# Optimization experiments

Hardware: AMD Instinct MI355X
Metric: run time of the kernel (lower is better)

## Reference

```python
import jax, jax.numpy as jnp
import numpy as np

B, L = 2, 2048
IN_DIM, HD_DIM, STATE_DIM = 512, 4096, 16
NUM_PATHS, ENT_DEPTH = 2, 2
ENT_STRENGTH, WALK_TIME = 0.3, 1.0


def _glorot(key, shape):
    lim = np.sqrt(6.0 / (shape[0] + shape[1]))
    return jax.random.uniform(key, shape, jnp.float32, -lim, lim)


def setup_inputs() -> dict:
    key = jax.random.key(0)
    ks = jax.random.split(key, 10)
    x = jax.random.normal(ks[0], (B, L, IN_DIM), jnp.float32)
    input_proj = _glorot(ks[1], (IN_DIM, HD_DIM))
    output_proj = _glorot(ks[2], (HD_DIM, IN_DIM))
    a_log = jax.random.uniform(ks[3], (STATE_DIM,), jnp.float32, -4.0, -1.0)
    b_proj = _glorot(ks[4], (HD_DIM, STATE_DIM))
    c_proj = _glorot(ks[5], (HD_DIM, STATE_DIM))
    dt_proj = jnp.full((HD_DIM,), 0.01, jnp.float32)
    skip_proj = jnp.ones((HD_DIM,), jnp.float32)  # diagonal skip, init 1.0
    amplitudes_real = jnp.full((NUM_PATHS,), 1.0 / np.sqrt(NUM_PATHS), jnp.float32)
    amplitudes_imag = 0.01 * jax.random.normal(ks[6], (NUM_PATHS,), jnp.float32)
    rotation_angles = jax.random.uniform(ks[7], (ENT_DEPTH, NUM_PATHS), jnp.float32, 0.0, 2.0 * np.pi)
    wh, _ = jnp.linalg.qr(jax.random.normal(ks[8], (NUM_PATHS, NUM_PATHS), jnp.float32))  # orthogonal init
    return dict(x=x, input_proj=input_proj, output_proj=output_proj, a_log=a_log,
                b_proj=b_proj, c_proj=c_proj, dt_proj=dt_proj, skip_proj=skip_proj,
                amplitudes_real=amplitudes_real, amplitudes_imag=amplitudes_imag,
                rotation_angles=rotation_angles, walk_hamiltonian=wh)


def _qhd_forward(x, input_proj, output_proj, a_log, b_proj, c_proj, dt_proj,
                 skip_proj, amp_r, amp_i, rot, walk_h):
    Bb, Ll, _ = x.shape
    K = amp_r.shape[0]
    dt = jax.nn.softplus(dt_proj)                                   # (D,)
    hd = jnp.einsum('bld,dh->blh', x, input_proj)                   # (B,L,D)
    # --- frequency-stratified superposition paths (K bands) ---
    Xf = jnp.fft.rfft(hd, axis=1)                                   # (B,F,D) complex
    F = Xf.shape[1]
    band = jnp.clip(jnp.arange(F) * K // F, 0, K - 1)
    masks = (band[None, :] == jnp.arange(K)[:, None]).astype(hd.dtype)  # (K,F)
    x_paths = jnp.fft.irfft(Xf[None] * masks[:, None, :, None], n=Ll, axis=2)  # (K,B,L,D)
    # --- FFT-domain diagonal selective SSM (causal conv with exp decay) ---
    a = -jnp.exp(a_log)                                             # (N,)
    dt_bar = jnp.mean(dt)
    t_idx = jnp.arange(Ll, dtype=hd.dtype)
    decay = jnp.exp(a[None, :] * dt_bar * t_idx[:, None])           # (L,N)
    Bt = jnp.einsum('kbld,dn->kbln', x_paths * dt, b_proj)          # (K,B,L,N)
    n2 = 2 * Ll
    h = jnp.fft.irfft(jnp.fft.rfft(Bt, n=n2, axis=2) * jnp.fft.rfft(decay, n=n2, axis=0),
                      n=n2, axis=2)[:, :, :Ll, :]                   # (K,B,L,N)
    y_paths = jnp.einsum('kbln,dn->kbld', h, c_proj)                # (K,B,L,D)
    # --- VQC entanglement (RY-style phase + quantum-walk mixing) ---
    alpha = amp_r.astype(jnp.complex64) + 1j * amp_i.astype(jnp.complex64)
    A = 1j * (ENT_STRENGTH * WALK_TIME) * walk_h.astype(jnp.complex64)
    U = jnp.eye(K, dtype=jnp.complex64) + A + (A @ A) / 2.0 + (A @ A @ A) / 6.0
    for d in range(rot.shape[0]):
        alpha = jnp.exp(1j * rot[d].astype(jnp.complex64)) * alpha
        alpha = U @ alpha
    # --- Born rule collapse ---
    w = jnp.abs(alpha) ** 2
    w = (w / jnp.sum(w)).astype(hd.dtype)                           # (K,)
    y = jnp.einsum('k,kbld->bld', w, y_paths) + hd * skip_proj      # diagonal skip
    return jnp.einsum('blh,hd->bld', y, output_proj)                # (B,L,in_dim)


def reference(x, input_proj, output_proj, a_log, b_proj, c_proj, dt_proj,
              skip_proj, amplitudes_real, amplitudes_imag, rotation_angles,
              walk_hamiltonian):
    return _qhd_forward(x, input_proj, output_proj, a_log, b_proj, c_proj,
                        dt_proj, skip_proj, amplitudes_real, amplitudes_imag,
                        rotation_angles, walk_hamiltonian)
```

## Files before the change

### kernel.cpp

```cpp
#include <hip/hip_runtime.h>
#include <cstdint>

typedef unsigned short ushort_t;
typedef __bf16 bf16x8 __attribute__((ext_vector_type(8)));
typedef float f32x4 __attribute__((ext_vector_type(4)));

#define PI_F 3.14159265358979323846f

__device__ __forceinline__ ushort_t f2bf(float f) {
  uint32_t x = __float_as_uint(f);
  x += 0x7fffu + ((x >> 16) & 1u);
  return (ushort_t)(x >> 16);
}
__device__ __forceinline__ float bf2f(ushort_t u) {
  return __uint_as_float(((uint32_t)u) << 16);
}
__device__ __forceinline__ float softplusf(float x) {
  return (x > 20.f) ? x : log1pf(expf(x));
}
__device__ __forceinline__ void async_ld16(ushort_t* lds, const ushort_t* g) {
  __builtin_amdgcn_global_load_lds(
      (const __attribute__((address_space(1))) uint32_t*)g,
      (__attribute__((address_space(3))) uint32_t*)lds, 16, 0, 0);
}
__device__ __forceinline__ void load16f(const float* p, float* v) {
  const float4* q = reinterpret_cast<const float4*>(p);
  float4 t0 = q[0], t1 = q[1], t2 = q[2], t3 = q[3];
  v[0]=t0.x; v[1]=t0.y; v[2]=t0.z; v[3]=t0.w;
  v[4]=t1.x; v[5]=t1.y; v[6]=t1.z; v[7]=t1.w;
  v[8]=t2.x; v[9]=t2.y; v[10]=t2.z; v[11]=t2.w;
  v[12]=t3.x; v[13]=t3.y; v[14]=t3.z; v[15]=t3.w;
}


__global__ __launch_bounds__(256) void cast_bf16(const float* __restrict__ in,
                                                 ushort_t* __restrict__ out, int n) {
  int i = blockIdx.x * 256 + threadIdx.x;
  if (i < n) out[i] = f2bf(in[i]);
}

__global__ __launch_bounds__(256) void zero_f4(float4* __restrict__ p) {
  int i = blockIdx.x * 256 + threadIdx.x;
  p[i] = (float4){0.f, 0.f, 0.f, 0.f};
}

__global__ __launch_bounds__(256) void transpose_cast(const float* __restrict__ in,
                                                      ushort_t* __restrict__ out,
                                                      int R, int C,
                                                      const float* __restrict__ scale) {
  __shared__ float t[32][33];
  int bc = blockIdx.x * 32;
  int br = blockIdx.y * 32;
  int tx = threadIdx.x, ty = threadIdx.y;
#pragma unroll
  for (int i = ty; i < 32; i += 8)
    t[i][tx] = in[(size_t)(br + i) * C + bc + tx];
  __syncthreads();
#pragma unroll
  for (int i = ty; i < 32; i += 8) {
    float sv = scale ? scale[bc + i] : 1.f;
    out[(size_t)(bc + i) * R + br + tx] = f2bf(t[tx][i] * sv);
  }
}

__global__ __launch_bounds__(256) void bdt_kernel(const float* __restrict__ bp,
                                                  const float* __restrict__ dtp,
                                                  float* __restrict__ bdt) {
  int i = blockIdx.x * 256 + threadIdx.x;
  bdt[i] = bp[i] * softplusf(dtp[i >> 4]);
}

__global__ __launch_bounds__(256) void small_setup(const float* __restrict__ dtp,
                                                   const float* __restrict__ a_log,
                                                   const float* __restrict__ ar,
                                                   const float* __restrict__ ai,
                                                   const float* __restrict__ rot,
                                                   const float* __restrict__ wh,
                                                   float* __restrict__ sc) {
  __shared__ float red[256];
  float s = 0.f;
  for (int i = threadIdx.x; i < 4096; i += 256) s += softplusf(dtp[i]);
  red[threadIdx.x] = s;
  __syncthreads();
  for (int st = 128; st > 0; st >>= 1) {
    if (threadIdx.x < st) red[threadIdx.x] += red[threadIdx.x + st];
    __syncthreads();
  }
  if (threadIdx.x == 0) {
    float dtbar = red[0] / 4096.f;
    float B00 = 0.3f * wh[0], B01 = 0.3f * wh[1], B10 = 0.3f * wh[2], B11 = 0.3f * wh[3];
    float C00 = B00*B00 + B01*B10, C01 = B00*B01 + B01*B11;
    float C10 = B10*B00 + B11*B10, C11 = B10*B01 + B11*B11;
    float D00 = C00*B00 + C01*B10, D01 = C00*B01 + C01*B11;
    float D10 = C10*B00 + C11*B10, D11 = C10*B01 + C11*B11;
    float Ur00 = 1.f - 0.5f*C00, Ur01 = -0.5f*C01, Ur10 = -0.5f*C10, Ur11 = 1.f - 0.5f*C11;
    float Ui00 = B00 - D00/6.f, Ui01 = B01 - D01/6.f, Ui10 = B10 - D10/6.f, Ui11 = B11 - D11/6.f;
    float a0r = ar[0], a0i = ai[0], a1r = ar[1], a1i = ai[1];
#pragma unroll
    for (int d = 0; d < 2; ++d) {
      float c0 = cosf(rot[d*2+0]), s0 = sinf(rot[d*2+0]);
      float c1 = cosf(rot[d*2+1]), s1 = sinf(rot[d*2+1]);
      float t0r = a0r*c0 - a0i*s0, t0i = a0r*s0 + a0i*c0;
      float t1r = a1r*c1 - a1i*s1, t1i = a1r*s1 + a1i*c1;
      a0r = Ur00*t0r - Ui00*t0i + Ur01*t1r - Ui01*t1i;
      a0i = Ur00*t0i + Ui00*t0r + Ur01*t1i + Ui01*t1r;
      a1r = Ur10*t0r - Ui10*t0i + Ur11*t1r - Ui11*t1i;
      a1i = Ur10*t0i + Ui10*t0r + Ur11*t1i + Ui11*t1r;
    }
    float p0 = a0r*a0r + a0i*a0i, p1 = a1r*a1r + a1i*a1i;
    float inv = 1.f / (p0 + p1);
    sc[0] = p0 * inv; sc[1] = p1 * inv; sc[2] = dtbar;
#pragma unroll
    for (int n = 0; n < 16; ++n) {
      float a = -expf(a_log[n]);
      sc[8 + n]  = expf(a * dtbar);
      sc[24 + n] = expf(a * dtbar * 32.f);
    }
  }
}


__global__ __launch_bounds__(256)
void skinny16(const float* __restrict__ A, const float* __restrict__ Bm,
              float* __restrict__ C, int K, int lda) {
  const int m0 = blockIdx.x << 2;
  const int tid = threadIdx.x;
  float acc[4][16];
#pragma unroll
  for (int a = 0; a < 4; ++a)
#pragma unroll
    for (int n = 0; n < 16; ++n) acc[a][n] = 0.f;

  for (int d = tid; d < K; d += 256) {
    float bv[16];
    load16f(Bm + (size_t)d * 16, bv);
    float av[4];
#pragma unroll
    for (int a = 0; a < 4; ++a) av[a] = A[(size_t)(m0 + a) * lda + d];
#pragma unroll
    for (int a = 0; a < 4; ++a)
#pragma unroll
      for (int n = 0; n < 16; ++n) acc[a][n] += av[a] * bv[n];
  }
  __shared__ float sred[4][4][16];
  const int w = tid >> 6, lane = tid & 63;
#pragma unroll
  for (int a = 0; a < 4; ++a)
#pragma unroll
    for (int n = 0; n < 16; ++n) {
      float v = acc[a][n];
#pragma unroll
      for (int off2 = 32; off2 > 0; off2 >>= 1) v += __shfl_down(v, off2);
      if (lane == 0) sred[w][a][n] = v;
    }
  __syncthreads();
  if (tid < 64) {
    int a = tid >> 4, n = tid & 15;
    C[(size_t)(m0 + a) * 16 + n] =
        sred[0][a][n] + sred[1][a][n] + sred[2][a][n] + sred[3][a][n];
  }
}


template<int BM, int BN, int WR, int WC, bool OBF, bool FUSE>
__global__ __launch_bounds__(256)
void gemm_bf16(const ushort_t* __restrict__ A, const ushort_t* __restrict__ Bt,
               void* __restrict__ Cv, int M, int N, int Kc, int lda, int ldb, int swz,
               const ushort_t* __restrict__ hb, const ushort_t* __restrict__ cp) {
  constexpr int BK = 64;
  constexpr int WMR = BM / WR;
  constexpr int WNC = BN / WC;
  constexpr int MI = WMR / 16;
  constexpr int NI = WNC / 16;
  constexpr int NCA = BM * BK * 2 / 1024;
  constexpr int NCB = BN * BK * 2 / 1024;

  __shared__ ushort_t lA[BM * BK];
  __shared__ ushort_t lB[BN * BK];

  const int tid = threadIdx.x;
  const int w = tid >> 6, lane = tid & 63;
  const int wr = w / WC, wc = w % WC;
  const int r = lane & 15, g = lane >> 4;

  const int nbx = gridDim.x;
  int bid = blockIdx.y * nbx + blockIdx.x;
  if (swz) {
    const int nwg = nbx * gridDim.y;
    bid = (bid & 7) * (nwg >> 3) + (bid >> 3);
  }
  const int m0 = (bid / nbx) * BM, n0 = (bid % nbx) * BN;
  const int kz = blockIdx.z * Kc;

  f32x4 acc[MI][NI];
#pragma unroll
  for (int mi = 0; mi < MI; ++mi)
#pragma unroll
    for (int ni = 0; ni < NI; ++ni)
      acc[mi][ni] = (f32x4){0.f, 0.f, 0.f, 0.f};

  const int ktiles = Kc >> 6;
  for (int kt = 0; kt < ktiles; ++kt) {
    const int k0 = kz + (kt << 6);
    for (int c = w; c < NCA; c += 4) {
      int byteoff = (c << 10) + (lane << 4);
      int row = byteoff >> 7;
      int scol = (byteoff & 127) ^ ((row & 7) << 4);
      async_ld16(&lA[c << 9], &A[(size_t)(m0 + row) * lda + k0 + (scol >> 1)]);
    }
    for (int c = w; c < NCB; c += 4) {
      int byteoff = (c << 10) + (lane << 4);
      int row = byteoff >> 7;
      int scol = (byteoff & 127) ^ ((row & 7) << 4);
      async_ld16(&lB[c << 9], &Bt[(size_t)(n0 + row) * ldb + k0 + (scol >> 1)]);
    }
    __syncthreads();
#pragma unroll
    for (int kk = 0; kk < 2; ++kk) {
      bf16x8 av[MI], bv[NI];
#pragma unroll
      for (int mi = 0; mi < MI; ++mi) {
        int row = wr * WMR + mi * 16 + r;
        int off = (((kk << 2) + g) ^ (row & 7)) << 3;
        av[mi] = *reinterpret_cast<const bf16x8*>(&lA[row * 64 + off]);
      }
#pragma unroll
      for (int ni = 0; ni < NI; ++ni) {
        int row = wc * WNC + ni * 16 + r;
        int off = (((kk << 2) + g) ^ (row & 7)) << 3;
        bv[ni] = *reinterpret_cast<const bf16x8*>(&lB[row * 64 + off]);
      }
#pragma unroll
      for (int mi = 0; mi < MI; ++mi)
#pragma unroll
        for (int ni = 0; ni < NI; ++ni)
          acc[mi][ni] = __builtin_amdgcn_mfma_f32_16x16x32_bf16(av[mi], bv[ni], acc[mi][ni], 0, 0, 0);
    }
    __syncthreads();
  }

  if constexpr (FUSE) {
    bf16x8 zv;
#pragma unroll
    for (int t2 = 0; t2 < 8; ++t2) zv[t2] = (__bf16)0.0f;
    bf16x8 ah[MI], bh[NI];
#pragma unroll
    for (int mi = 0; mi < MI; ++mi) {
      ah[mi] = zv;
      if (g < 2) {
        int row = m0 + wr * WMR + mi * 16 + r;
        ah[mi] = *reinterpret_cast<const bf16x8*>(&hb[(size_t)row * 16 + g * 8]);
      }
    }
#pragma unroll
    for (int ni = 0; ni < NI; ++ni) {
      bh[ni] = zv;
      if (g < 2) {
        int col = n0 + wc * WNC + ni * 16 + r;
        bh[ni] = *reinterpret_cast<const bf16x8*>(&cp[(size_t)col * 16 + g * 8]);
      }
    }
#pragma unroll
    for (int mi = 0; mi < MI; ++mi)
#pragma unroll
      for (int ni = 0; ni < NI; ++ni)
        acc[mi][ni] = __builtin_amdgcn_mfma_f32_16x16x32_bf16(ah[mi], bh[ni], acc[mi][ni], 0, 0, 0);
  }

#pragma unroll
  for (int mi = 0; mi < MI; ++mi)
#pragma unroll
    for (int ni = 0; ni < NI; ++ni) {
      int row = m0 + wr * WMR + mi * 16 + g * 4;
      int col = n0 + wc * WNC + ni * 16 + r;
#pragma unroll
      for (int j = 0; j < 4; ++j) {
        size_t idx = (size_t)(row + j) * N + col;
        if (OBF) ((ushort_t*)Cv)[idx] = f2bf(acc[mi][ni][j]);
        else     unsafeAtomicAdd(&((float*)Cv)[idx], acc[mi][ni][j]);
      }
    }
}


__global__ __launch_bounds__(256)
void freq_ssm(const float* __restrict__ Bhd, const float* __restrict__ sc,
              ushort_t* __restrict__ h) {
  const int blk = blockIdx.x;
  const int b = blk >> 4, n = blk & 15;
  const int tid = threadIdx.x;
  __shared__ float2 X[2048];
  __shared__ float carr[64], pre[64];
  const float w0 = sc[0], w1 = sc[1];
  const float r = sc[8 + n], r32 = sc[24 + n];

  for (int l = tid; l < 2048; l += 256) {
    X[l].x = Bhd[(size_t)(b * 2048 + l) * 16 + n];
    X[l].y = 0.f;
  }
  for (int ls = 10; ls >= 0; --ls) {
    int s = 1 << ls;
    __syncthreads();
    for (int q = tid; q < 1024; q += 256) {
      int j = q & (s - 1);
      int base = (q >> ls) << (ls + 1);
      int i0 = base + j, i1 = i0 + s;
      float2 a = X[i0], bb = X[i1];
      X[i0].x = a.x + bb.x; X[i0].y = a.y + bb.y;
      float tx = a.x - bb.x, ty = a.y - bb.y;
      float ang = -PI_F * (float)j / (float)s;
      float sn, cs; sincosf(ang, &sn, &cs);
      X[i1].x = tx * cs - ty * sn;
      X[i1].y = tx * sn + ty * cs;
    }
  }
  __syncthreads();
  for (int i = tid; i < 2048; i += 256) {
    unsigned f = __brev((unsigned)i) >> 21;
    float wv = (f <= 512u || f >= 1536u) ? w0 : w1;
    X[i].x *= wv; X[i].y *= wv;
  }
  for (int ls = 0; ls <= 10; ++ls) {
    int s = 1 << ls;
    __syncthreads();
    for (int q = tid; q < 1024; q += 256) {
      int j = q & (s - 1);
      int base = (q >> ls) << (ls + 1);
      int i0 = base + j, i1 = i0 + s;
      float ang = PI_F * (float)j / (float)s;
      float sn, cs; sincosf(ang, &sn, &cs);
      float2 bb = X[i1];
      float bx = bb.x * cs - bb.y * sn;
      float by = bb.x * sn + bb.y * cs;
      float2 a = X[i0];
      X[i0].x = a.x + bx; X[i0].y = a.y + by;
      X[i1].x = a.x - bx; X[i1].y = a.y - by;
    }
  }
  __syncthreads();
  const float inv = 1.0f / 2048.0f;
  if (tid < 64) {
    float c = 0.f;
    int base = tid * 32;
#pragma unroll
    for (int i = 0; i < 32; ++i) c = r * c + X[base + i].x * inv;
    carr[tid] = c;
  }
  __syncthreads();
  if (tid == 0) {
    float s = 0.f;
    for (int j2 = 0; j2 < 64; ++j2) { pre[j2] = s; s = s * r32 + carr[j2]; }
  }
  __syncthreads();
  if (tid < 64) {
    float s = pre[tid];
    int base = tid * 32;
#pragma unroll
    for (int i = 0; i < 32; ++i) {
      s = r * s + X[base + i].x * inv;
      h[(size_t)(b * 2048 + base + i) * 16 + n] = f2bf(s);
    }
  }
}


extern "C" void kernel_launch(void* const* d_in, const int* in_sizes, int n_in,
                              void* d_out, int out_size, void* d_ws, size_t ws_size,
                              hipStream_t stream) {
  (void)in_sizes; (void)n_in; (void)out_size; (void)ws_size;
  const float* x      = (const float*)d_in[0];
  const float* Win    = (const float*)d_in[1];
  const float* Wout   = (const float*)d_in[2];
  const float* a_log  = (const float*)d_in[3];
  const float* b_proj = (const float*)d_in[4];
  const float* c_proj = (const float*)d_in[5];
  const float* dt_proj= (const float*)d_in[6];
  const float* skip   = (const float*)d_in[7];
  const float* ampr   = (const float*)d_in[8];
  const float* ampi   = (const float*)d_in[9];
  const float* rot    = (const float*)d_in[10];
  const float* wh     = (const float*)d_in[11];
  float* out = (float*)d_out;

  char* ws = (char*)d_ws;
  ushort_t* A1  = (ushort_t*)(ws + 0);
  ushort_t* Wt1 = (ushort_t*)(ws + 4194304);
  ushort_t* Wt2 = (ushort_t*)(ws + 8388608);
  float*    bdt = (float*)(ws + 12582912);
  float*    Wb  = (float*)(ws + 12845056);
  float*    Bhd = (float*)(ws + 12910592);
  ushort_t* hb  = (ushort_t*)(ws + 13172736);
  ushort_t* cp16= (ushort_t*)(ws + 13303808);
  float*    sc  = (float*)(ws + 13434880);
  ushort_t* y   = (ushort_t*)(ws + 13435136);

  zero_f4<<<2048, 256, 0, stream>>>((float4*)out);
  cast_bf16<<<8192, 256, 0, stream>>>(x, A1, 4096 * 512);
  cast_bf16<<<256, 256, 0, stream>>>(c_proj, cp16, 65536);
  transpose_cast<<<dim3(128, 16), dim3(32, 8), 0, stream>>>(Win, Wt1, 512, 4096, skip);
  transpose_cast<<<dim3(16, 128), dim3(32, 8), 0, stream>>>(Wout, Wt2, 4096, 512, nullptr);
  bdt_kernel<<<256, 256, 0, stream>>>(b_proj, dt_proj, bdt);
  small_setup<<<1, 256, 0, stream>>>(dt_proj, a_log, ampr, ampi, rot, wh, sc);

  skinny16<<<128, 256, 0, stream>>>(Win, bdt, Wb, 4096, 4096);
  skinny16<<<1024, 256, 0, stream>>>(x, Wb, Bhd, 512, 512);
  freq_ssm<<<32, 256, 0, stream>>>(Bhd, sc, hb);

  gemm_bf16<128, 128, 2, 2, true, true><<<dim3(32, 32), 256, 0, stream>>>(
      A1, Wt1, y, 4096, 4096, 512, 512, 512, 1, hb, cp16);

  gemm_bf16<64, 128, 1, 4, false, false><<<dim3(4, 64, 4), 256, 0, stream>>>(
      y, Wt2, out, 4096, 512, 1024, 4096, 4096, 1, nullptr, nullptr);
}
```

Before: 261.6 us.

## Replace split-K atomics with partial buffers, fuse bdt, table FFT twiddles

The final split-K GEMM now writes plain stores into four partial buffers, and a separate reduceK kernel sums them into the output. This replaces both the zero-fill kernel and the atomic adds. The bdt scaling is folded into a new skinny16_bdt kernel, removing one launch. freq_ssm now runs with 512 threads and reads precomputed twiddles from an LDS table instead of calling sincosf in every butterfly. The cost is an extra 32 MB of partial-buffer traffic plus one added reduction launch.

```diff
diff --git a/kernel.cpp b/kernel.cpp
--- a/kernel.cpp
+++ b/kernel.cpp
@@ -37,11 +37,6 @@
                                                  ushort_t* __restrict__ out, int n) {
   int i = blockIdx.x * 256 + threadIdx.x;
   if (i < n) out[i] = f2bf(in[i]);
-}
-
-__global__ __launch_bounds__(256) void zero_f4(float4* __restrict__ p) {
-  int i = blockIdx.x * 256 + threadIdx.x;
-  p[i] = (float4){0.f, 0.f, 0.f, 0.f};
 }
 
 __global__ __launch_bounds__(256) void transpose_cast(const float* __restrict__ in,
@@ -61,13 +56,6 @@
     float sv = scale ? scale[bc + i] : 1.f;
     out[(size_t)(bc + i) * R + br + tx] = f2bf(t[tx][i] * sv);
   }
-}
-
-__global__ __launch_bounds__(256) void bdt_kernel(const float* __restrict__ bp,
-                                                  const float* __restrict__ dtp,
-                                                  float* __restrict__ bdt) {
-  int i = blockIdx.x * 256 + threadIdx.x;
-  bdt[i] = bp[i] * softplusf(dtp[i >> 4]);
 }
 
 __global__ __launch_bounds__(256) void small_setup(const float* __restrict__ dtp,
@@ -137,6 +125,52 @@
     float av[4];
 #pragma unroll
     for (int a = 0; a < 4; ++a) av[a] = A[(size_t)(m0 + a) * lda + d];
+#pragma unroll
+    for (int a = 0; a < 4; ++a)
+#pragma unroll
+      for (int n = 0; n < 16; ++n) acc[a][n] += av[a] * bv[n];
+  }
+  __shared__ float sred[4][4][16];
+  const int w = tid >> 6, lane = tid & 63;
+#pragma unroll
+  for (int a = 0; a < 4; ++a)
+#pragma unroll
+    for (int n = 0; n < 16; ++n) {
+      float v = acc[a][n];
+#pragma unroll
+      for (int off2 = 32; off2 > 0; off2 >>= 1) v += __shfl_down(v, off2);
+      if (lane == 0) sred[w][a][n] = v;
+    }
+  __syncthreads();
+  if (tid < 64) {
+    int a = tid >> 4, n = tid & 15;
+    C[(size_t)(m0 + a) * 16 + n] =
+        sred[0][a][n] + sred[1][a][n] + sred[2][a][n] + sred[3][a][n];
+  }
+}
+
+
+__global__ __launch_bounds__(256)
+void skinny16_bdt(const float* __restrict__ A, const float* __restrict__ bp,
+                  const float* __restrict__ dtp, float* __restrict__ C,
+                  int K, int lda) {
+  const int m0 = blockIdx.x << 2;
+  const int tid = threadIdx.x;
+  float acc[4][16];
+#pragma unroll
+  for (int a = 0; a < 4; ++a)
+#pragma unroll
+    for (int n = 0; n < 16; ++n) acc[a][n] = 0.f;
+
+  for (int d = tid; d < K; d += 256) {
+    float bv[16];
+    load16f(bp + (size_t)d * 16, bv);
+    float sp = softplusf(dtp[d]);
+    float av[4];
+#pragma unroll
+    for (int a = 0; a < 4; ++a) av[a] = A[(size_t)(m0 + a) * lda + d];
+#pragma unroll
+    for (int n = 0; n < 16; ++n) bv[n] *= sp;
 #pragma unroll
     for (int a = 0; a < 4; ++a)
 #pragma unroll
@@ -267,6 +301,7 @@
         acc[mi][ni] = __builtin_amdgcn_mfma_f32_16x16x32_bf16(ah[mi], bh[ni], acc[mi][ni], 0, 0, 0);
   }
 
+  const size_t zoff = (size_t)blockIdx.z * (size_t)M * (size_t)N;
 #pragma unroll
   for (int mi = 0; mi < MI; ++mi)
 #pragma unroll
@@ -275,47 +310,68 @@
       int col = n0 + wc * WNC + ni * 16 + r;
 #pragma unroll
       for (int j = 0; j < 4; ++j) {
-        size_t idx = (size_t)(row + j) * N + col;
+        size_t idx = zoff + (size_t)(row + j) * N + col;
         if (OBF) ((ushort_t*)Cv)[idx] = f2bf(acc[mi][ni][j]);
-        else     unsafeAtomicAdd(&((float*)Cv)[idx], acc[mi][ni][j]);
+        else     ((float*)Cv)[idx]   = acc[mi][ni][j];
       }
     }
 }
 
 
 __global__ __launch_bounds__(256)
+void reduceK(const float4* __restrict__ p, float4* __restrict__ out) {
+  int i = blockIdx.x * 256 + threadIdx.x;
+  float4 a = p[i];
+  float4 b = p[i + 524288];
+  float4 c = p[i + 1048576];
+  float4 d = p[i + 1572864];
+  float4 o;
+  o.x = a.x + b.x + c.x + d.x;
+  o.y = a.y + b.y + c.y + d.y;
+  o.z = a.z + b.z + c.z + d.z;
+  o.w = a.w + b.w + c.w + d.w;
+  out[i] = o;
+}
+
+
+__global__ __launch_bounds__(512)
 void freq_ssm(const float* __restrict__ Bhd, const float* __restrict__ sc,
               ushort_t* __restrict__ h) {
   const int blk = blockIdx.x;
   const int b = blk >> 4, n = blk & 15;
   const int tid = threadIdx.x;
   __shared__ float2 X[2048];
+  __shared__ float2 TW[1024];
   __shared__ float carr[64], pre[64];
   const float w0 = sc[0], w1 = sc[1];
   const float r = sc[8 + n], r32 = sc[24 + n];
 
-  for (int l = tid; l < 2048; l += 256) {
+  for (int l = tid; l < 2048; l += 512) {
     X[l].x = Bhd[(size_t)(b * 2048 + l) * 16 + n];
     X[l].y = 0.f;
+  }
+  for (int k = tid; k < 1024; k += 512) {
+    float sn, cs;
+    sincosf(PI_F * (float)k * (1.0f / 1024.0f), &sn, &cs);
+    TW[k].x = cs; TW[k].y = sn;
   }
   for (int ls = 10; ls >= 0; --ls) {
     int s = 1 << ls;
     __syncthreads();
-    for (int q = tid; q < 1024; q += 256) {
+    for (int q = tid; q < 1024; q += 512) {
       int j = q & (s - 1);
       int base = (q >> ls) << (ls + 1);
       int i0 = base + j, i1 = i0 + s;
       float2 a = X[i0], bb = X[i1];
       X[i0].x = a.x + bb.x; X[i0].y = a.y + bb.y;
       float tx = a.x - bb.x, ty = a.y - bb.y;
-      float ang = -PI_F * (float)j / (float)s;
-      float sn, cs; sincosf(ang, &sn, &cs);
-      X[i1].x = tx * cs - ty * sn;
-      X[i1].y = tx * sn + ty * cs;
-    }
-  }
-  __syncthreads();
-  for (int i = tid; i < 2048; i += 256) {
+      float2 t = TW[j << (10 - ls)];
+      X[i1].x = tx * t.x + ty * t.y;
+      X[i1].y = ty * t.x - tx * t.y;
+    }
+  }
+  __syncthreads();
+  for (int i = tid; i < 2048; i += 512) {
     unsigned f = __brev((unsigned)i) >> 21;
     float wv = (f <= 512u || f >= 1536u) ? w0 : w1;
     X[i].x *= wv; X[i].y *= wv;
@@ -323,15 +379,14 @@
   for (int ls = 0; ls <= 10; ++ls) {
     int s = 1 << ls;
     __syncthreads();
-    for (int q = tid; q < 1024; q += 256) {
+    for (int q = tid; q < 1024; q += 512) {
       int j = q & (s - 1);
       int base = (q >> ls) << (ls + 1);
       int i0 = base + j, i1 = i0 + s;
-      float ang = PI_F * (float)j / (float)s;
-      float sn, cs; sincosf(ang, &sn, &cs);
+      float2 t = TW[j << (10 - ls)];
       float2 bb = X[i1];
-      float bx = bb.x * cs - bb.y * sn;
-      float by = bb.x * sn + bb.y * cs;
+      float bx = bb.x * t.x - bb.y * t.y;
+      float by = bb.x * t.y + bb.y * t.x;
       float2 a = X[i0];
       X[i0].x = a.x + bx; X[i0].y = a.y + by;
       X[i1].x = a.x - bx; X[i1].y = a.y - by;
@@ -386,29 +441,28 @@
   ushort_t* A1  = (ushort_t*)(ws + 0);
   ushort_t* Wt1 = (ushort_t*)(ws + 4194304);
   ushort_t* Wt2 = (ushort_t*)(ws + 8388608);
-  float*    bdt = (float*)(ws + 12582912);
-  float*    Wb  = (float*)(ws + 12845056);
-  float*    Bhd = (float*)(ws + 12910592);
-  ushort_t* hb  = (ushort_t*)(ws + 13172736);
-  ushort_t* cp16= (ushort_t*)(ws + 13303808);
-  float*    sc  = (float*)(ws + 13434880);
-  ushort_t* y   = (ushort_t*)(ws + 13435136);
-
-  zero_f4<<<2048, 256, 0, stream>>>((float4*)out);
+  float*    Wb  = (float*)(ws + 12582912);
+  float*    Bhd = (float*)(ws + 12615680);
+  ushort_t* hb  = (ushort_t*)(ws + 12877824);
+  ushort_t* cp16= (ushort_t*)(ws + 13008896);
+  float*    sc  = (float*)(ws + 13139968);
+  ushort_t* y   = (ushort_t*)(ws + 13140224);
+  float*    part= (float*)(ws + 46694656);
+
   cast_bf16<<<8192, 256, 0, stream>>>(x, A1, 4096 * 512);
   cast_bf16<<<256, 256, 0, stream>>>(c_proj, cp16, 65536);
   transpose_cast<<<dim3(128, 16), dim3(32, 8), 0, stream>>>(Win, Wt1, 512, 4096, skip);
   transpose_cast<<<dim3(16, 128), dim3(32, 8), 0, stream>>>(Wout, Wt2, 4096, 512, nullptr);
-  bdt_kernel<<<256, 256, 0, stream>>>(b_proj, dt_proj, bdt);
   small_setup<<<1, 256, 0, stream>>>(dt_proj, a_log, ampr, ampi, rot, wh, sc);
 
-  skinny16<<<128, 256, 0, stream>>>(Win, bdt, Wb, 4096, 4096);
+  skinny16_bdt<<<128, 256, 0, stream>>>(Win, b_proj, dt_proj, Wb, 4096, 4096);
   skinny16<<<1024, 256, 0, stream>>>(x, Wb, Bhd, 512, 512);
-  freq_ssm<<<32, 256, 0, stream>>>(Bhd, sc, hb);
+  freq_ssm<<<32, 512, 0, stream>>>(Bhd, sc, hb);
 
   gemm_bf16<128, 128, 2, 2, true, true><<<dim3(32, 32), 256, 0, stream>>>(
       A1, Wt1, y, 4096, 4096, 512, 512, 512, 1, hb, cp16);
 
   gemm_bf16<64, 128, 1, 4, false, false><<<dim3(4, 64, 4), 256, 0, stream>>>(
-      y, Wt2, out, 4096, 512, 1024, 4096, 4096, 1, nullptr, nullptr);
-}
+      y, Wt2, part, 4096, 512, 1024, 4096, 4096, 1, nullptr, nullptr);
+  reduceK<<<2048, 256, 0, stream>>>((const float4*)part, (float4*)out);
+}
```

Result: faster. 242.9 us (-7.2%).
